# Kernel optimization log

Hardware: AMD Instinct MI355X
Metric: run time of the kernel (lower is better)

Reference implementation:

```python
import jax, jax.numpy as jnp
import numpy as np

NUM_HEADS = 16
KERNEL_SIZE = 13


def setup_inputs() -> dict:
    key = jax.random.key(0)
    ks = jax.random.split(key, 6)
    B, L, C = 4, 4096, 512
    H, K = NUM_HEADS, KERNEL_SIZE
    x = jax.random.normal(ks[0], (B, L, C), dtype=jnp.float32)
    qkv_w = jax.random.normal(ks[1], (C, 3 * C), dtype=jnp.float32) * 0.02
    qkv_b = jnp.zeros((3 * C,), dtype=jnp.float32)
    rpb = jax.random.normal(ks[2], (H, 2 * K - 1), dtype=jnp.float32) * 0.02
    proj_w = jax.random.normal(ks[3], (C, C), dtype=jnp.float32) * 0.02
    proj_b = jnp.zeros((C,), dtype=jnp.float32)
    return {"x": x, "qkv_w": qkv_w, "qkv_b": qkv_b, "rpb": rpb,
            "proj_w": proj_w, "proj_b": proj_b}


def reference(x, qkv_w, qkv_b, rpb, proj_w, proj_b):
    B, L, C = x.shape
    H, K = NUM_HEADS, KERNEL_SIZE
    hd = C // H
    scale = hd ** -0.5
    kh = K // 2

    # qkv projection -> q,k,v each [B,H,L,hd]
    qkv = (x @ qkv_w + qkv_b).reshape(B, L, 3, H, hd).transpose(2, 0, 3, 1, 4)
    q, k, v = qkv[0] * scale, qkv[1], qkv[2]

    # NATTEN window: start index clamped so window stays in-bounds
    pos = jnp.arange(L)
    ni = jnp.clip(pos - kh, 0, L - K)              # [L] window start per query
    idx = ni[:, None] + jnp.arange(K)[None, :]     # [L,K] key positions
    # rpb index: (key_pos - query_pos) + (K-1)
    rpb_idx = (ni - pos + (K - 1))[:, None] + jnp.arange(K)[None, :]  # [L,K]

    k_win = k[:, :, idx, :]                        # [B,H,L,K,hd]
    v_win = v[:, :, idx, :]                        # [B,H,L,K,hd]

    attn = jnp.einsum('bhld,bhlkd->bhlk', q, k_win) + rpb[:, rpb_idx][None]
    attn = jax.nn.softmax(attn, axis=-1)

    out = jnp.einsum('bhlk,bhlkd->bhld', attn, v_win)  # [B,H,L,hd]
    out = out.transpose(0, 2, 1, 3).reshape(B, L, C)
    return out @ proj_w + proj_b
```

## Files before the change

### kernel.cpp

```cpp
#include <hip/hip_runtime.h>
#include <hip/hip_bf16.h>
#include <stdint.h>


typedef __attribute__((ext_vector_type(8))) short short8;
typedef __attribute__((ext_vector_type(4))) float f32x4;
typedef __attribute__((ext_vector_type(8))) unsigned short u16x8;
typedef __attribute__((ext_vector_type(4))) float float4v;

#define NB 4
#define NL 4096
#define NC 512
#define NH 16
#define HD 32
#define KW 13
#define KHALF 6
#define NM (NB*NL)

__device__ __forceinline__ float b2f(unsigned short u) {
  union { unsigned int i; float f; } x; x.i = ((unsigned int)u) << 16; return x.f;
}
__device__ __forceinline__ unsigned short f2b(float f) {
  __hip_bfloat16 h = __float2bfloat16(f);
  return __builtin_bit_cast(unsigned short, h);
}
__device__ __forceinline__ void gll16(const unsigned short* g, unsigned short* l) {
  __builtin_amdgcn_global_load_lds(
      (const __attribute__((address_space(1))) void*)g,
      (__attribute__((address_space(3))) void*)l, 16, 0, 0);
}

__global__ __launch_bounds__(256) void cvt_f32_bf16(const float* __restrict__ in,
                                                    unsigned short* __restrict__ out) {
  long i = (long)blockIdx.x * 256 + threadIdx.x;
  const float4v* in4 = (const float4v*)in;
  float4v a = in4[i * 2];
  float4v b = in4[i * 2 + 1];
  u16x8 u;
  u[0] = f2b(a.x); u[1] = f2b(a.y); u[2] = f2b(a.z); u[3] = f2b(a.w);
  u[4] = f2b(b.x); u[5] = f2b(b.y); u[6] = f2b(b.z); u[7] = f2b(b.w);
  ((u16x8*)out)[i] = u;
}

__global__ __launch_bounds__(256)
void pack_bf(const float* __restrict__ W, unsigned short* __restrict__ Bf,
             int N, int ngroups) {
  int g = blockIdx.x * 256 + threadIdx.x;
  if (g >= ngroups) return;
  int lane = g & 63;
  int kb   = (g >> 6) & 1;
  int nj   = (g >> 7) & 3;
  int wn   = (g >> 9) & 1;
  int kt   = (g >> 10) & 7;
  int tn   = g >> 13;
  int n  = tn * 128 + wn * 64 + nj * 16 + (lane & 15);
  int k0 = kt * 64 + (kb * 4 + (lane >> 4)) * 8;
  u16x8 u;
  #pragma unroll
  for (int e = 0; e < 8; ++e) u[e] = f2b(W[(long)(k0 + e) * N + n]);
  ((u16x8*)Bf)[g] = u;
}


__device__ __forceinline__ void stage_tileA(const unsigned short* __restrict__ G,
                                            long rowBase, int K, int kt,
                                            unsigned short* ldsDst, int tid) {
  int r  = tid >> 3;
  int ch = (tid & 7) ^ (r & 7);
  const unsigned short* s0 = G + (rowBase + r) * (long)K + kt * 64 + ch * 8;
  unsigned short* d0 = ldsDst + tid * 8;
  #pragma unroll
  for (int q = 0; q < 4; ++q)
    gll16(s0 + (long)32 * q * K, d0 + 2048 * q);
}

#define BAR() __builtin_amdgcn_s_barrier()
#define LGK0() do { asm volatile("s_waitcnt lgkmcnt(0)" ::: "memory"); \
                    __builtin_amdgcn_sched_barrier(0); } while (0)
#define VM(N) asm volatile("s_waitcnt vmcnt(" #N ")" ::: "memory")

#define LDA(ABASE) do { \
  const char* _ba = (const char*)(ABASE); \
  _Pragma("unroll") for (int ii = 0; ii < 4; ++ii) { \
    int _row = wm*64 + ii*16 + lr; \
    _Pragma("unroll") for (int kb = 0; kb < 2; ++kb) \
      af[ii][kb] = *(const short8*)(_ba + _row*128 + (((kb*4+lk) ^ lr7) * 16)); \
  } \
} while (0)

#define LDBG(KT) do { \
  const short8* _bp = (const short8*)(Bfw + (long)(KT) * 8192) + lane; \
  _Pragma("unroll") for (int nj = 0; nj < 4; ++nj) \
    _Pragma("unroll") for (int kb = 0; kb < 2; ++kb) \
      bf[nj][kb] = _bp[(nj*2 + kb) * 64]; \
} while (0)

#define MMA_ALL() do { \
  __builtin_amdgcn_s_setprio(1); \
  _Pragma("unroll") for (int ii = 0; ii < 4; ++ii) \
    _Pragma("unroll") for (int jj = 0; jj < 4; ++jj) \
      _Pragma("unroll") for (int kb = 0; kb < 2; ++kb) \
        acc[ii][jj] = __builtin_amdgcn_mfma_f32_16x16x32_bf16( \
            af[ii][kb], bf[jj][kb], acc[ii][jj], 0, 0, 0); \
  __builtin_amdgcn_s_setprio(0); \
} while (0)

#define GTILE(ABUF, KT, STG, VMARG) do { \
  LDBG(KT); \
  LDA(ABUF); \
  LGK0(); \
  BAR(); \
  if (STG) stage_tileA(Ag, mBase, K, (KT) + 2, ABUF, tid); \
  VMARG; \
  MMA_ALL(); \
  BAR(); \
} while (0)

template<int OUT_BF16>
__global__ __launch_bounds__(256, 3)
void gemm128(const unsigned short* __restrict__ Ag,
             const unsigned short* __restrict__ Bf,
             const float* __restrict__ bias,
             void* __restrict__ Cout,
             int M, int N, int K, int tilesN) {
  __shared__ __align__(16) unsigned short lds[16384];

  int tid = threadIdx.x;
  int nwg = gridDim.x;
  int cpx = nwg >> 3;
  int wg  = ((int)blockIdx.x & 7) * cpx + ((int)blockIdx.x >> 3);
  int tm = wg / tilesN, tn = wg % tilesN;
  long mBase = (long)tm * 128;
  long nBase = (long)tn * 128;

  int lane = tid & 63, wave = tid >> 6;
  int wm = wave >> 1;
  int wn = wave & 1;
  int lr = lane & 15, lk = lane >> 4, lr7 = lr & 7;

  const unsigned short* Bfw = Bf + (long)tn * 65536 + wn * 4096;

  unsigned short* A0 = lds;
  unsigned short* A1 = lds + 8192;

  f32x4 acc[4][4];
  #pragma unroll
  for (int i = 0; i < 4; ++i)
    #pragma unroll
    for (int j = 0; j < 4; ++j) acc[i][j] = (f32x4){0.f, 0.f, 0.f, 0.f};

  short8 af[4][2], bf[4][2];

  stage_tileA(Ag, mBase, K, 0, A0, tid);
  stage_tileA(Ag, mBase, K, 1, A1, tid);
  VM(4);
  BAR();

  #pragma unroll 1
  for (int i = 0; i < 3; ++i) {
    GTILE(A0, 2*i,     true, VM(4));
    GTILE(A1, 2*i + 1, true, VM(4));
  }
  GTILE(A0, 6, false, VM(0));
  GTILE(A1, 7, false, VM(0));

  long rowb = mBase + wm * 64 + (lane >> 4) * 4;
  int  colb = (int)nBase + wn * 64 + lr;
  if (OUT_BF16) {
    unsigned short* C = (unsigned short*)Cout;
    #pragma unroll
    for (int mi = 0; mi < 4; ++mi)
      #pragma unroll
      for (int nj = 0; nj < 4; ++nj) {
        int col = colb + nj * 16;
        float bv = bias[col];
        #pragma unroll
        for (int r = 0; r < 4; ++r)
          C[(rowb + mi * 16 + r) * (long)N + col] = f2b(acc[mi][nj][r] + bv);
      }
  } else {
    float* C = (float*)Cout;
    #pragma unroll
    for (int mi = 0; mi < 4; ++mi)
      #pragma unroll
      for (int nj = 0; nj < 4; ++nj) {
        int col = colb + nj * 16;
        float bv = bias[col];
        #pragma unroll
        for (int r = 0; r < 4; ++r)
          C[(rowb + mi * 16 + r) * (long)N + col] = acc[mi][nj][r] + bv;
      }
  }
}

__global__ __launch_bounds__(256)
void natt(const unsigned short* __restrict__ qkv, const float* __restrict__ rpb,
          unsigned short* __restrict__ out) {
  int tid = blockIdx.x * 256 + threadIdx.x;
  int h = tid & 15;
  int l = (tid >> 4) & (NL - 1);
  int b = tid >> 16;
  const float scale = 0.17677669529663687f;

  long qb = ((long)(b * NL + l) * 3) * NC + h * HD;
  float q[HD];
  {
    const u16x8* q8 = (const u16x8*)(qkv + qb);
    #pragma unroll
    for (int w = 0; w < 4; ++w) {
      u16x8 u = q8[w];
      #pragma unroll
      for (int e = 0; e < 8; ++e) q[w * 8 + e] = b2f(u[e]) * scale;
    }
  }

  int ni = l - KHALF;
  if (ni < 0) ni = 0;
  if (ni > NL - KW) ni = NL - KW;
  const float* rb = rpb + h * (2 * KW - 1) + (ni - l + KW - 1);

  float p[KW];
  float mx = -1e30f;
  #pragma unroll
  for (int j = 0; j < KW; ++j) {
    long kb = ((long)(b * NL + ni + j) * 3 + 1) * NC + h * HD;
    const u16x8* k8 = (const u16x8*)(qkv + kb);
    float s = 0.f;
    #pragma unroll
    for (int w = 0; w < 4; ++w) {
      u16x8 u = k8[w];
      #pragma unroll
      for (int e = 0; e < 8; ++e) s += q[w * 8 + e] * b2f(u[e]);
    }
    s += rb[j];
    p[j] = s;
    mx = fmaxf(mx, s);
  }

  float sum = 0.f;
  #pragma unroll
  for (int j = 0; j < KW; ++j) { p[j] = __expf(p[j] - mx); sum += p[j]; }
  float inv = 1.0f / sum;

  float o[HD];
  #pragma unroll
  for (int d = 0; d < HD; ++d) o[d] = 0.f;
  #pragma unroll
  for (int j = 0; j < KW; ++j) {
    long vb = ((long)(b * NL + ni + j) * 3 + 2) * NC + h * HD;
    const u16x8* v8 = (const u16x8*)(qkv + vb);
    float wj = p[j] * inv;
    #pragma unroll
    for (int w = 0; w < 4; ++w) {
      u16x8 u = v8[w];
      #pragma unroll
      for (int e = 0; e < 8; ++e) o[w * 8 + e] += wj * b2f(u[e]);
    }
  }

  unsigned short* op = out + (long)(b * NL + l) * NC + h * HD;
  #pragma unroll
  for (int w = 0; w < 4; ++w) {
    u16x8 u;
    #pragma unroll
    for (int e = 0; e < 8; ++e) u[e] = f2b(o[w * 8 + e]);
    *((u16x8*)(op + w * 8)) = u;
  }
}

extern "C" void kernel_launch(void* const* d_in, const int* in_sizes, int n_in,
                              void* d_out, int out_size, void* d_ws, size_t ws_size,
                              hipStream_t stream) {
  const float* x      = (const float*)d_in[0];
  const float* qkv_w  = (const float*)d_in[1];
  const float* qkv_b  = (const float*)d_in[2];
  const float* rpb    = (const float*)d_in[3];
  const float* proj_w = (const float*)d_in[4];
  const float* proj_b = (const float*)d_in[5];
  float* out = (float*)d_out;

  char* ws = (char*)d_ws;
  unsigned short* xb   = (unsigned short*)(ws);
  unsigned short* Bf1  = (unsigned short*)(ws + 16777216);
  unsigned short* Bf2  = (unsigned short*)(ws + 18350080);
  unsigned short* qkvo = (unsigned short*)(ws + 18874368);
  unsigned short* attno= (unsigned short*)(ws + 69206016);

  cvt_f32_bf16<<<dim3(4096), dim3(256), 0, stream>>>(x, xb);
  pack_bf<<<dim3(384), dim3(256), 0, stream>>>(qkv_w, Bf1, 1536, 98304);
  pack_bf<<<dim3(128), dim3(256), 0, stream>>>(proj_w, Bf2, 512, 32768);
  gemm128<1><<<dim3(1536), dim3(256), 0, stream>>>(xb, Bf1, qkv_b, qkvo,
                                                   NM, 1536, 512, 12);
  natt<<<dim3(1024), dim3(256), 0, stream>>>(qkvo, rpb, attno);
  gemm128<0><<<dim3(512), dim3(256), 0, stream>>>(attno, Bf2, proj_b, out,
                                                  NM, 512, 512, 4);
}
```

Before: 97.41 us.

## Merge conversion/pack kernels and retile GEMM waves to 32x128 strips

Combines the x conversion and the two weight-packing kernels into a single launch to cut launch overhead. It also changes the GEMM wave layout from a 2x2 grid of 64x64 sub-tiles to four waves each owning 32 rows by the full 128 columns. The B-fragment packing is changed to match. Each wave now loads all of B from global memory per k-step, so it holds more B registers and fewer A fragments, and launch bounds drop to 2 blocks per CU. This trades more B traffic and register pressure for less LDS A-reading per wave.

```diff
diff --git a/kernel.cpp b/kernel.cpp
--- a/kernel.cpp
+++ b/kernel.cpp
@@ -24,42 +24,52 @@
   __hip_bfloat16 h = __float2bfloat16(f);
   return __builtin_bit_cast(unsigned short, h);
 }
-__device__ __forceinline__ void gll16(const unsigned short* g, unsigned short* l) {
+__device__ __forceinline__ void gll16(const void* g, unsigned short* l) {
   __builtin_amdgcn_global_load_lds(
       (const __attribute__((address_space(1))) void*)g,
       (__attribute__((address_space(3))) void*)l, 16, 0, 0);
 }
 
-__global__ __launch_bounds__(256) void cvt_f32_bf16(const float* __restrict__ in,
-                                                    unsigned short* __restrict__ out) {
-  long i = (long)blockIdx.x * 256 + threadIdx.x;
-  const float4v* in4 = (const float4v*)in;
-  float4v a = in4[i * 2];
-  float4v b = in4[i * 2 + 1];
-  u16x8 u;
-  u[0] = f2b(a.x); u[1] = f2b(a.y); u[2] = f2b(a.z); u[3] = f2b(a.w);
-  u[4] = f2b(b.x); u[5] = f2b(b.y); u[6] = f2b(b.z); u[7] = f2b(b.w);
-  ((u16x8*)out)[i] = u;
-}
-
-__global__ __launch_bounds__(256)
-void pack_bf(const float* __restrict__ W, unsigned short* __restrict__ Bf,
-             int N, int ngroups) {
-  int g = blockIdx.x * 256 + threadIdx.x;
-  if (g >= ngroups) return;
+__device__ __forceinline__ void pack_one(const float* __restrict__ W,
+                                         unsigned short* __restrict__ Bf,
+                                         int N, int g) {
   int lane = g & 63;
   int kb   = (g >> 6) & 1;
-  int nj   = (g >> 7) & 3;
-  int wn   = (g >> 9) & 1;
+  int nj   = (g >> 7) & 7;
   int kt   = (g >> 10) & 7;
   int tn   = g >> 13;
-  int n  = tn * 128 + wn * 64 + nj * 16 + (lane & 15);
+  int n  = tn * 128 + nj * 16 + (lane & 15);
   int k0 = kt * 64 + (kb * 4 + (lane >> 4)) * 8;
   u16x8 u;
   #pragma unroll
   for (int e = 0; e < 8; ++e) u[e] = f2b(W[(long)(k0 + e) * N + n]);
   ((u16x8*)Bf)[g] = u;
 }
+__global__ __launch_bounds__(256)
+void cvt_and_pack(const float* __restrict__ x, unsigned short* __restrict__ xb,
+                  const float* __restrict__ W1, unsigned short* __restrict__ Bf1,
+                  const float* __restrict__ W2, unsigned short* __restrict__ Bf2) {
+  int bid = blockIdx.x;
+  if (bid < 4096) {
+    long i = (long)bid * 256 + threadIdx.x;
+    const float4v* in4 = (const float4v*)x;
+    float4v a = in4[i * 2];
+    float4v b = in4[i * 2 + 1];
+    u16x8 u;
+    u[0] = f2b(a.x); u[1] = f2b(a.y); u[2] = f2b(a.z); u[3] = f2b(a.w);
+    u[4] = f2b(b.x); u[5] = f2b(b.y); u[6] = f2b(b.z); u[7] = f2b(b.w);
+    ((u16x8*)xb)[i] = u;
+  } else {
+    int g = (bid - 4096) * 256 + threadIdx.x;
+    if (g < 98304) pack_one(W1, Bf1, 1536, g);
+    else           pack_one(W2, Bf2, 512, g - 98304);
+  }
+}
+
+#define BAR() __builtin_amdgcn_s_barrier()
+#define LGK0() do { asm volatile("s_waitcnt lgkmcnt(0)" ::: "memory"); \
+                    __builtin_amdgcn_sched_barrier(0); } while (0)
+#define VM(N) asm volatile("s_waitcnt vmcnt(" #N ")" ::: "memory")
 
 
 __device__ __forceinline__ void stage_tileA(const unsigned short* __restrict__ G,
@@ -74,15 +84,10 @@
     gll16(s0 + (long)32 * q * K, d0 + 2048 * q);
 }
 
-#define BAR() __builtin_amdgcn_s_barrier()
-#define LGK0() do { asm volatile("s_waitcnt lgkmcnt(0)" ::: "memory"); \
-                    __builtin_amdgcn_sched_barrier(0); } while (0)
-#define VM(N) asm volatile("s_waitcnt vmcnt(" #N ")" ::: "memory")
-
-#define LDA(ABASE) do { \
+#define LDA_B16(ABASE) do { \
   const char* _ba = (const char*)(ABASE); \
-  _Pragma("unroll") for (int ii = 0; ii < 4; ++ii) { \
-    int _row = wm*64 + ii*16 + lr; \
+  _Pragma("unroll") for (int ii = 0; ii < 2; ++ii) { \
+    int _row = wave*32 + ii*16 + lr; \
     _Pragma("unroll") for (int kb = 0; kb < 2; ++kb) \
       af[ii][kb] = *(const short8*)(_ba + _row*128 + (((kb*4+lk) ^ lr7) * 16)); \
   } \
@@ -90,24 +95,24 @@
 
 #define LDBG(KT) do { \
   const short8* _bp = (const short8*)(Bfw + (long)(KT) * 8192) + lane; \
-  _Pragma("unroll") for (int nj = 0; nj < 4; ++nj) \
+  _Pragma("unroll") for (int nj = 0; nj < 8; ++nj) \
     _Pragma("unroll") for (int kb = 0; kb < 2; ++kb) \
       bf[nj][kb] = _bp[(nj*2 + kb) * 64]; \
 } while (0)
 
 #define MMA_ALL() do { \
   __builtin_amdgcn_s_setprio(1); \
-  _Pragma("unroll") for (int ii = 0; ii < 4; ++ii) \
-    _Pragma("unroll") for (int jj = 0; jj < 4; ++jj) \
+  _Pragma("unroll") for (int ii = 0; ii < 2; ++ii) \
+    _Pragma("unroll") for (int nj = 0; nj < 8; ++nj) \
       _Pragma("unroll") for (int kb = 0; kb < 2; ++kb) \
-        acc[ii][jj] = __builtin_amdgcn_mfma_f32_16x16x32_bf16( \
-            af[ii][kb], bf[jj][kb], acc[ii][jj], 0, 0, 0); \
+        acc[ii][nj] = __builtin_amdgcn_mfma_f32_16x16x32_bf16( \
+            af[ii][kb], bf[nj][kb], acc[ii][nj], 0, 0, 0); \
   __builtin_amdgcn_s_setprio(0); \
 } while (0)
 
 #define GTILE(ABUF, KT, STG, VMARG) do { \
   LDBG(KT); \
-  LDA(ABUF); \
+  LDA_B16(ABUF); \
   LGK0(); \
   BAR(); \
   if (STG) stage_tileA(Ag, mBase, K, (KT) + 2, ABUF, tid); \
@@ -117,7 +122,7 @@
 } while (0)
 
 template<int OUT_BF16>
-__global__ __launch_bounds__(256, 3)
+__global__ __launch_bounds__(256, 2)
 void gemm128(const unsigned short* __restrict__ Ag,
              const unsigned short* __restrict__ Bf,
              const float* __restrict__ bias,
@@ -134,22 +139,20 @@
   long nBase = (long)tn * 128;
 
   int lane = tid & 63, wave = tid >> 6;
-  int wm = wave >> 1;
-  int wn = wave & 1;
   int lr = lane & 15, lk = lane >> 4, lr7 = lr & 7;
 
-  const unsigned short* Bfw = Bf + (long)tn * 65536 + wn * 4096;
+  const unsigned short* Bfw = Bf + (long)tn * 65536;
 
   unsigned short* A0 = lds;
   unsigned short* A1 = lds + 8192;
 
-  f32x4 acc[4][4];
-  #pragma unroll
-  for (int i = 0; i < 4; ++i)
-    #pragma unroll
-    for (int j = 0; j < 4; ++j) acc[i][j] = (f32x4){0.f, 0.f, 0.f, 0.f};
-
-  short8 af[4][2], bf[4][2];
+  f32x4 acc[2][8];
+  #pragma unroll
+  for (int i = 0; i < 2; ++i)
+    #pragma unroll
+    for (int j = 0; j < 8; ++j) acc[i][j] = (f32x4){0.f, 0.f, 0.f, 0.f};
+
+  short8 af[2][2], bf[8][2];
 
   stage_tileA(Ag, mBase, K, 0, A0, tid);
   stage_tileA(Ag, mBase, K, 1, A1, tid);
@@ -164,14 +167,14 @@
   GTILE(A0, 6, false, VM(0));
   GTILE(A1, 7, false, VM(0));
 
-  long rowb = mBase + wm * 64 + (lane >> 4) * 4;
-  int  colb = (int)nBase + wn * 64 + lr;
+  long rowb = mBase + wave * 32 + (lane >> 4) * 4;
+  int  colb = (int)nBase + lr;
   if (OUT_BF16) {
     unsigned short* C = (unsigned short*)Cout;
     #pragma unroll
-    for (int mi = 0; mi < 4; ++mi)
-      #pragma unroll
-      for (int nj = 0; nj < 4; ++nj) {
+    for (int mi = 0; mi < 2; ++mi)
+      #pragma unroll
+      for (int nj = 0; nj < 8; ++nj) {
         int col = colb + nj * 16;
         float bv = bias[col];
         #pragma unroll
@@ -181,9 +184,9 @@
   } else {
     float* C = (float*)Cout;
     #pragma unroll
-    for (int mi = 0; mi < 4; ++mi)
-      #pragma unroll
-      for (int nj = 0; nj < 4; ++nj) {
+    for (int mi = 0; mi < 2; ++mi)
+      #pragma unroll
+      for (int nj = 0; nj < 8; ++nj) {
         int col = colb + nj * 16;
         float bv = bias[col];
         #pragma unroll
@@ -286,9 +289,8 @@
   unsigned short* qkvo = (unsigned short*)(ws + 18874368);
   unsigned short* attno= (unsigned short*)(ws + 69206016);
 
-  cvt_f32_bf16<<<dim3(4096), dim3(256), 0, stream>>>(x, xb);
-  pack_bf<<<dim3(384), dim3(256), 0, stream>>>(qkv_w, Bf1, 1536, 98304);
-  pack_bf<<<dim3(128), dim3(256), 0, stream>>>(proj_w, Bf2, 512, 32768);
+  cvt_and_pack<<<dim3(4608), dim3(256), 0, stream>>>(x, xb, qkv_w, Bf1,
+                                                     proj_w, Bf2);
   gemm128<1><<<dim3(1536), dim3(256), 0, stream>>>(xb, Bf1, qkv_b, qkvo,
                                                    NM, 1536, 512, 12);
   natt<<<dim3(1024), dim3(256), 0, stream>>>(qkvo, rpb, attno);
```

New measurement: 107.2 us. 10.0% more time.
